# Kernel tuning notes

Measured on AMD Instinct MI355X. Metric: run time of the kernel, lower is better.

## Reference

```python
import jax, jax.numpy as jnp
import numpy as np

N_EMBD = 1024
N_HEAD = 16
HEAD_SIZE = N_EMBD // N_HEAD
B, T = 4, 2048
LN_EPS = 1e-6  # flax.linen.LayerNorm default


def _layer_norm(x, scale, bias):
    mu = jnp.mean(x, axis=-1, keepdims=True)
    var = jnp.mean(jnp.square(x - mu), axis=-1, keepdims=True)
    return (x - mu) * jax.lax.rsqrt(var + LN_EPS) * scale + bias


def setup_inputs() -> dict:
    key = jax.random.key(0)
    ks = jax.random.split(key, 12)
    s_in = 1.0 / np.sqrt(N_EMBD)
    s_ff = 1.0 / np.sqrt(4 * N_EMBD)
    return {
        "x": jax.random.normal(ks[0], (B, T, N_EMBD), jnp.float32),
        "wq": jax.random.normal(ks[1], (N_HEAD, N_EMBD, HEAD_SIZE), jnp.float32) * s_in,
        "wk": jax.random.normal(ks[2], (N_HEAD, N_EMBD, HEAD_SIZE), jnp.float32) * s_in,
        "wv": jax.random.normal(ks[3], (N_HEAD, N_EMBD, HEAD_SIZE), jnp.float32) * s_in,
        "w_proj": jax.random.normal(ks[4], (N_EMBD, N_EMBD), jnp.float32) * s_in,
        "b_proj": jnp.zeros((N_EMBD,), jnp.float32),
        "ln1_scale": jnp.ones((N_EMBD,), jnp.float32),
        "ln1_bias": jnp.zeros((N_EMBD,), jnp.float32),
        "ln2_scale": jnp.ones((N_EMBD,), jnp.float32),
        "ln2_bias": jnp.zeros((N_EMBD,), jnp.float32),
        "w1": jax.random.normal(ks[5], (N_EMBD, 4 * N_EMBD), jnp.float32) * s_in,
        "b1": jnp.zeros((4 * N_EMBD,), jnp.float32),
        "w2": jax.random.normal(ks[6], (4 * N_EMBD, N_EMBD), jnp.float32) * s_ff,
        "b2": jnp.zeros((N_EMBD,), jnp.float32),
    }


def reference(x, wq, wk, wv, w_proj, b_proj, ln1_scale, ln1_bias,
              ln2_scale, ln2_bias, w1, b1, w2, b2):
    Bb, Tt, C = x.shape
    # --- pre-LN self-attention ---
    h = _layer_norm(x, ln1_scale, ln1_bias)
    q = jnp.einsum('btc,hcd->bhtd', h, wq)
    k = jnp.einsum('btc,hcd->bhtd', h, wk)
    v = jnp.einsum('btc,hcd->bhtd', h, wv)
    # NOTE: original scales by C**-0.5 with C = full embed dim (quirk preserved)
    wei = jnp.einsum('bhtd,bhsd->bhts', q, k) * (C ** -0.5)
    tril = jnp.tril(jnp.ones((Tt, Tt), dtype=bool))
    wei = jnp.where(tril, wei, -jnp.inf)
    wei = jax.nn.softmax(wei, axis=-1)
    attn = jnp.einsum('bhts,bhsd->bhtd', wei, v)  # (B,H,T,hd)
    attn = attn.transpose(0, 2, 1, 3).reshape(Bb, Tt, -1)  # concat heads
    x = x + attn @ w_proj + b_proj
    # --- pre-LN feed-forward (dropout deterministic -> identity) ---
    h2 = _layer_norm(x, ln2_scale, ln2_bias)
    x = x + jax.nn.relu(h2 @ w1 + b1) @ w2 + b2
    return x
```

## Files before the change

kernel.cpp:

```cpp
#include <hip/hip_runtime.h>
#include <hip/hip_bf16.h>

#define BB 4
#define TT 2048
#define CC 1024
#define HH 16
#define DD 64
#define FF 4096
#define MM (BB*TT)

typedef __attribute__((ext_vector_type(4))) float  f32x4;
typedef __attribute__((ext_vector_type(8))) __bf16 bf16x8v;
typedef __attribute__((ext_vector_type(4))) short  s16x4;
typedef __attribute__((ext_vector_type(8))) short  s16x8;
typedef __attribute__((ext_vector_type(4))) unsigned short u16x4;

__device__ inline unsigned short bf16bits(float f){
  __hip_bfloat16 h = __float2bfloat16(f);
  return __builtin_bit_cast(unsigned short, h);
}
__device__ inline bf16x8v as_bf16x8(s16x8 s){ return __builtin_bit_cast(bf16x8v, s); }

__device__ inline void gload_lds16(const void* g, void* l){
  __builtin_amdgcn_global_load_lds((const __attribute__((address_space(1))) void*)g,
                                   (__attribute__((address_space(3))) void*)l, 16, 0, 0);
}

__global__ __launch_bounds__(256) void transpose_cast(const float* __restrict__ in,
                                                      unsigned short* __restrict__ out,
                                                      int K, int N){
  __shared__ float tile[32][33];
  int n0 = blockIdx.x*32, k0 = blockIdx.y*32;
  int tx = threadIdx.x, ty = threadIdx.y;
#pragma unroll
  for (int i=0;i<32;i+=8) tile[ty+i][tx] = in[(size_t)(k0+ty+i)*N + n0+tx];
  __syncthreads();
#pragma unroll
  for (int i=0;i<32;i+=8)
    out[(size_t)(n0+ty+i)*K + k0+tx] = bf16bits(tile[tx][ty+i]);
}

__global__ __launch_bounds__(256) void tcast_qkv(const float* __restrict__ wq,
                                                 const float* __restrict__ wk,
                                                 const float* __restrict__ wv,
                                                 unsigned short* __restrict__ out){
  int z = blockIdx.z; int sel = z>>4; int h = z&15;
  const float* w = (sel==0)?wq:((sel==1)?wk:wv);
  const float* in = w + (size_t)h*CC*DD;
  unsigned short* o = out + (size_t)(sel*1024 + h*64)*CC;
  __shared__ float tile[32][33];
  int d0 = blockIdx.x*32, c0 = blockIdx.y*32;
  int tx = threadIdx.x, ty = threadIdx.y;
#pragma unroll
  for (int i=0;i<32;i+=8) tile[ty+i][tx] = in[(size_t)(c0+ty+i)*DD + d0+tx];
  __syncthreads();
#pragma unroll
  for (int i=0;i<32;i+=8)
    o[(size_t)(d0+ty+i)*CC + c0+tx] = bf16bits(tile[tx][ty+i]);
}

__global__ __launch_bounds__(256) void ln_kernel(const float* __restrict__ x,
                                                 const float* __restrict__ sc,
                                                 const float* __restrict__ bi,
                                                 unsigned short* __restrict__ out){
  __shared__ float red[4];
  const int row = blockIdx.x, tid = threadIdx.x;
  const float4 xv = ((const float4*)(x + (size_t)row*CC))[tid];
  float s = xv.x + xv.y + xv.z + xv.w;
#pragma unroll
  for (int m=32;m>=1;m>>=1) s += __shfl_xor(s, m);
  if ((tid&63)==0) red[tid>>6] = s;
  __syncthreads();
  s = red[0]+red[1]+red[2]+red[3];
  const float mu = s * (1.0f/1024.0f);
  const float d0=xv.x-mu, d1=xv.y-mu, d2=xv.z-mu, d3=xv.w-mu;
  float sq = d0*d0 + d1*d1 + d2*d2 + d3*d3;
  __syncthreads();
#pragma unroll
  for (int m=32;m>=1;m>>=1) sq += __shfl_xor(sq, m);
  if ((tid&63)==0) red[tid>>6] = sq;
  __syncthreads();
  sq = red[0]+red[1]+red[2]+red[3];
  const float inv = rsqrtf(sq*(1.0f/1024.0f) + 1e-6f);
  const float4 scv = ((const float4*)sc)[tid];
  const float4 biv = ((const float4*)bi)[tid];
  u16x4 o;
  o[0] = bf16bits(d0*inv*scv.x + biv.x);
  o[1] = bf16bits(d1*inv*scv.y + biv.y);
  o[2] = bf16bits(d2*inv*scv.z + biv.z);
  o[3] = bf16bits(d3*inv*scv.w + biv.w);
  ((u16x4*)(out + (size_t)row*CC))[tid] = o;
}

template<int EPI>
__global__ __launch_bounds__(256) void gemm_bf16(
    const unsigned short* __restrict__ A, const unsigned short* __restrict__ Bt,
    void* __restrict__ Cout, const float* __restrict__ bias,
    const float* __restrict__ resid, int M, int N, int K)
{
  __shared__ unsigned short smem[8192];
  const int tid = threadIdx.x;
  const int lane = tid & 63, w = tid >> 6;
  const int m0 = blockIdx.y * 128, n0 = blockIdx.x * 128;
  const int wr = w >> 1, wc = w & 1;
  const int g = lane >> 4, q = lane & 15;
  f32x4 acc[4][4] = {};

  for (int k0 = 0; k0 < K; k0 += 32){
    __syncthreads();
#pragma unroll
    for (int i=0;i<2;i++){
      const int chunk = w*2 + i;
      const int row = chunk*16 + (lane>>2);
      const int ce  = (lane&3)*8;
      gload_lds16(A  + (size_t)(m0+row)*K + k0 + ce, (void*)&smem[chunk*512]);
      gload_lds16(Bt + (size_t)(n0+row)*K + k0 + ce, (void*)&smem[4096 + chunk*512]);
    }
    __syncthreads();
    bf16x8v af[4], bfr[4];
#pragma unroll
    for (int m=0;m<4;m++) af[m]  = as_bf16x8(*(const s16x8*)&smem[(wr*64 + m*16 + q)*32 + g*8]);
#pragma unroll
    for (int n=0;n<4;n++) bfr[n] = as_bf16x8(*(const s16x8*)&smem[4096 + (wc*64 + n*16 + q)*32 + g*8]);
#pragma unroll
    for (int m=0;m<4;m++)
#pragma unroll
      for (int n=0;n<4;n++)
        acc[m][n] = __builtin_amdgcn_mfma_f32_16x16x32_bf16(af[m], bfr[n], acc[m][n], 0,0,0);
  }

#pragma unroll
  for (int m=0;m<4;m++)
#pragma unroll
    for (int n=0;n<4;n++){
      const int col = n0 + wc*64 + n*16 + q;
#pragma unroll
      for (int r=0;r<4;r++){
        const int row = m0 + wr*64 + m*16 + g*4 + r;
        float v = acc[m][n][r];
        if (EPI==0){
          ((unsigned short*)Cout)[(size_t)row*N + col] = bf16bits(v);
        } else if (EPI==1 || EPI==3){
          v += bias[col] + resid[(size_t)row*N + col];
          ((float*)Cout)[(size_t)row*N + col] = v;
        } else {
          v += bias[col];
          v = fmaxf(v, 0.0f);
          ((unsigned short*)Cout)[(size_t)row*N + col] = bf16bits(v);
        }
      }
    }
}

__global__ __launch_bounds__(64) void attn_kernel(const unsigned short* __restrict__ qkv,
                                                  unsigned short* __restrict__ outc){
  const int lane = threadIdx.x;
  const int q0 = blockIdx.x*16;
  const int bh = blockIdx.y; const int b = bh>>4, h = bh&15;
  const int g = lane>>4, qq = lane&15;
  const size_t base = (size_t)(b*TT)*3072;
  const int qcol = h*64, kcol = 1024 + h*64, vcol = 2048 + h*64;

  s16x8 qf0, qf1;
  {
    const unsigned short* qp = qkv + base + (size_t)(q0+qq)*3072 + qcol + g*8;
    qf0 = *(const s16x8*)(qp);
    qf1 = *(const s16x8*)(qp + 32);
  }

  float m_i = -INFINITY, l_i = 0.0f;
  f32x4 ot[4] = {};

  for (int s0 = 0; s0 <= q0; s0 += 16){
    const unsigned short* kp = qkv + base + (size_t)(s0+qq)*3072 + kcol + g*8;
    s16x8 kf0 = *(const s16x8*)(kp);
    s16x8 kf1 = *(const s16x8*)(kp + 32);
    f32x4 st = {};
    st = __builtin_amdgcn_mfma_f32_16x16x32_bf16(as_bf16x8(kf0), as_bf16x8(qf0), st, 0,0,0);
    st = __builtin_amdgcn_mfma_f32_16x16x32_bf16(as_bf16x8(kf1), as_bf16x8(qf1), st, 0,0,0);
    float sv[4]; float pm = -INFINITY;
#pragma unroll
    for (int r=0;r<4;r++){
      const int s_abs = s0 + g*4 + r;
      float v = st[r] * 0.03125f;
      if (s_abs > q0 + qq) v = -INFINITY;
      sv[r] = v;
      pm = fmaxf(pm, v);
    }
    pm = fmaxf(pm, __shfl_xor(pm, 16));
    pm = fmaxf(pm, __shfl_xor(pm, 32));
    const float m_new = fmaxf(m_i, pm);
    const float alpha = __expf(m_i - m_new);
    float p[4]; float ps = 0.0f;
#pragma unroll
    for (int r=0;r<4;r++){ p[r] = __expf(sv[r] - m_new); ps += p[r]; }
    ps += __shfl_xor(ps, 16);
    ps += __shfl_xor(ps, 32);
    l_i = l_i*alpha + ps;
    s16x4 pb;
#pragma unroll
    for (int r=0;r<4;r++) pb[r] = (short)bf16bits(p[r]);
#pragma unroll
    for (int mb=0;mb<4;mb++){
      ot[mb] *= alpha;
      s16x4 vf;
#pragma unroll
      for (int j=0;j<4;j++){
        const int s_abs = s0 + g*4 + j;
        vf[j] = (short)qkv[base + (size_t)s_abs*3072 + vcol + mb*16 + qq];
      }
      ot[mb] = __builtin_amdgcn_mfma_f32_16x16x16bf16_1k(vf, pb, ot[mb], 0,0,0);
    }
    m_i = m_new;
  }

  const float inv = 1.0f / l_i;
#pragma unroll
  for (int mb=0;mb<4;mb++){
    u16x4 o;
#pragma unroll
    for (int r=0;r<4;r++) o[r] = bf16bits(ot[mb][r] * inv);
    *(u16x4*)&outc[(size_t)(b*TT + q0 + qq)*1024 + h*64 + mb*16 + g*4] = o;
  }
}

extern "C" void kernel_launch(void* const* d_in, const int* in_sizes, int n_in,
                              void* d_out, int out_size, void* d_ws, size_t ws_size,
                              hipStream_t stream)
{
  const float* x   = (const float*)d_in[0];
  const float* wq  = (const float*)d_in[1];
  const float* wk  = (const float*)d_in[2];
  const float* wv  = (const float*)d_in[3];
  const float* wpr = (const float*)d_in[4];
  const float* bpr = (const float*)d_in[5];
  const float* l1s = (const float*)d_in[6];
  const float* l1b = (const float*)d_in[7];
  const float* l2s = (const float*)d_in[8];
  const float* l2b = (const float*)d_in[9];
  const float* w1  = (const float*)d_in[10];
  const float* b1  = (const float*)d_in[11];
  const float* w2  = (const float*)d_in[12];
  const float* b2  = (const float*)d_in[13];
  float* out = (float*)d_out;

  char* ws = (char*)d_ws;
  unsigned short* qkv   = (unsigned short*)(ws + 0);
  unsigned short* hb    = (unsigned short*)(ws + 50331648);
  unsigned short* attnc = (unsigned short*)(ws + 67108864);
  float*          x1    = (float*)        (ws + 83886080);
  unsigned short* h2    = attnc;
  unsigned short* act   = (unsigned short*)(ws + 0);
  unsigned short* wqkvt = (unsigned short*)(ws + 117440512);
  unsigned short* wprt  = (unsigned short*)(ws + 123731968);
  unsigned short* w1t   = (unsigned short*)(ws + 125829120);
  unsigned short* w2t   = (unsigned short*)(ws + 134217728);

  tcast_qkv<<<dim3(2,32,48), dim3(32,8), 0, stream>>>(wq, wk, wv, wqkvt);
  transpose_cast<<<dim3(32,32),  dim3(32,8), 0, stream>>>(wpr, wprt, 1024, 1024);
  transpose_cast<<<dim3(128,32), dim3(32,8), 0, stream>>>(w1,  w1t,  1024, 4096);
  transpose_cast<<<dim3(32,128), dim3(32,8), 0, stream>>>(w2,  w2t,  4096, 1024);

  ln_kernel<<<MM, 256, 0, stream>>>(x, l1s, l1b, hb);
  gemm_bf16<0><<<dim3(24,64), 256, 0, stream>>>(hb, wqkvt, qkv, nullptr, nullptr, MM, 3072, 1024);
  attn_kernel<<<dim3(TT/16, BB*HH), 64, 0, stream>>>(qkv, attnc);
  gemm_bf16<1><<<dim3(8,64), 256, 0, stream>>>(attnc, wprt, x1, bpr, x, MM, 1024, 1024);
  ln_kernel<<<MM, 256, 0, stream>>>(x1, l2s, l2b, h2);
  gemm_bf16<2><<<dim3(32,64), 256, 0, stream>>>(h2, w1t, act, b1, nullptr, MM, 4096, 1024);
  gemm_bf16<3><<<dim3(8,64), 256, 0, stream>>>(act, w2t, out, b2, x1, MM, 1024, 4096);
}
```

Baseline: 722.1 us.

## Write V transposed from QKV GEMM, widen attention blocks, swizzle GEMM grids

The QKV GEMM epilogue now writes Q and K into a 2048-wide buffer and V transposed per batch (feature-major), so attention can load V fragments as contiguous 4-element vectors instead of scalar strided gathers. The attention kernel uses 4 waves per block (64 queries) and processes 64 keys per softmax step, amortising max/sum reductions and rescaling across four key blocks. All GEMMs get an XCD-aware block-index swizzle to improve L2 locality across chiplets. The transposed V stores are 8-byte scattered writes, which may cost some epilogue bandwidth.

```diff
diff --git a/kernel.cpp b/kernel.cpp
--- a/kernel.cpp
+++ b/kernel.cpp
@@ -92,16 +92,26 @@
   ((u16x4*)(out + (size_t)row*CC))[tid] = o;
 }
 
-template<int EPI>
+template<int EPI, int SWZ>
 __global__ __launch_bounds__(256) void gemm_bf16(
     const unsigned short* __restrict__ A, const unsigned short* __restrict__ Bt,
     void* __restrict__ Cout, const float* __restrict__ bias,
-    const float* __restrict__ resid, int M, int N, int K)
+    const float* __restrict__ resid, unsigned short* __restrict__ vT,
+    int M, int N, int K)
 {
   __shared__ unsigned short smem[8192];
   const int tid = threadIdx.x;
   const int lane = tid & 63, w = tid >> 6;
-  const int m0 = blockIdx.y * 128, n0 = blockIdx.x * 128;
+  int bx = blockIdx.x, by = blockIdx.y;
+  if (SWZ){
+    const int gx = gridDim.x;
+    const int nwg = gx * gridDim.y;
+    const int flat = bx + by*gx;
+    const int cpx = nwg >> 3;
+    const int orig = (flat & 7)*cpx + (flat >> 3);
+    bx = orig % gx; by = orig / gx;
+  }
+  const int m0 = by * 128, n0 = bx * 128;
   const int wr = w >> 1, wc = w & 1;
   const int g = lane >> 4, q = lane & 15;
   f32x4 acc[4][4] = {};
@@ -134,82 +144,112 @@
 #pragma unroll
     for (int n=0;n<4;n++){
       const int col = n0 + wc*64 + n*16 + q;
-#pragma unroll
-      for (int r=0;r<4;r++){
-        const int row = m0 + wr*64 + m*16 + g*4 + r;
-        float v = acc[m][n][r];
-        if (EPI==0){
-          ((unsigned short*)Cout)[(size_t)row*N + col] = bf16bits(v);
-        } else if (EPI==1 || EPI==3){
-          v += bias[col] + resid[(size_t)row*N + col];
-          ((float*)Cout)[(size_t)row*N + col] = v;
-        } else {
-          v += bias[col];
-          v = fmaxf(v, 0.0f);
-          ((unsigned short*)Cout)[(size_t)row*N + col] = bf16bits(v);
+      const int row0 = m0 + wr*64 + m*16 + g*4;
+      if (EPI==4 && n0 >= 2048){
+        const int c = col - 2048;
+        const int bq = row0 >> 11, t0 = row0 & 2047;
+        u16x4 o;
+#pragma unroll
+        for (int r=0;r<4;r++) o[r] = bf16bits(acc[m][n][r]);
+        *(u16x4*)&vT[((size_t)(bq*1024 + c))*2048 + t0] = o;
+      } else {
+#pragma unroll
+        for (int r=0;r<4;r++){
+          const int row = row0 + r;
+          float v = acc[m][n][r];
+          if (EPI==4){
+            ((unsigned short*)Cout)[(size_t)row*2048 + col] = bf16bits(v);
+          } else if (EPI==1 || EPI==3){
+            v += bias[col] + resid[(size_t)row*N + col];
+            ((float*)Cout)[(size_t)row*N + col] = v;
+          } else {
+            v += bias[col];
+            v = fmaxf(v, 0.0f);
+            ((unsigned short*)Cout)[(size_t)row*N + col] = bf16bits(v);
+          }
         }
       }
     }
 }
 
-__global__ __launch_bounds__(64) void attn_kernel(const unsigned short* __restrict__ qkv,
-                                                  unsigned short* __restrict__ outc){
-  const int lane = threadIdx.x;
-  const int q0 = blockIdx.x*16;
-  const int bh = blockIdx.y; const int b = bh>>4, h = bh&15;
-  const int g = lane>>4, qq = lane&15;
-  const size_t base = (size_t)(b*TT)*3072;
-  const int qcol = h*64, kcol = 1024 + h*64, vcol = 2048 + h*64;
-
-  s16x8 qf0, qf1;
-  {
-    const unsigned short* qp = qkv + base + (size_t)(q0+qq)*3072 + qcol + g*8;
-    qf0 = *(const s16x8*)(qp);
-    qf1 = *(const s16x8*)(qp + 32);
-  }
+__global__ __launch_bounds__(256) void attn_v2(const unsigned short* __restrict__ qk,
+                                               const unsigned short* __restrict__ vT,
+                                               unsigned short* __restrict__ outc){
+  const int flat = blockIdx.x + blockIdx.y*32;
+  const int orig = (flat & 7)*256 + (flat >> 3);
+  const int qt = orig & 31;
+  const int bh = orig >> 5;
+  const int b = bh >> 4, h = bh & 15;
+  const int w = threadIdx.x >> 6, lane = threadIdx.x & 63;
+  const int g = lane >> 4, qq = lane & 15;
+  const int q0 = qt*64 + w*16;
+  const size_t base = (size_t)b*TT*2048;
+
+  const unsigned short* qrow = qk + base + (size_t)(q0+qq)*2048 + h*64 + g*8;
+  const s16x8 qf0 = *(const s16x8*)qrow;
+  const s16x8 qf1 = *(const s16x8*)(qrow + 32);
+  const unsigned short* kbase = qk + base + 1024 + h*64 + g*8;
+  const size_t vbase = ((size_t)(b*1024 + h*64 + qq))*2048 + g*4;
 
   float m_i = -INFINITY, l_i = 0.0f;
   f32x4 ot[4] = {};
-
-  for (int s0 = 0; s0 <= q0; s0 += 16){
-    const unsigned short* kp = qkv + base + (size_t)(s0+qq)*3072 + kcol + g*8;
-    s16x8 kf0 = *(const s16x8*)(kp);
-    s16x8 kf1 = *(const s16x8*)(kp + 32);
-    f32x4 st = {};
-    st = __builtin_amdgcn_mfma_f32_16x16x32_bf16(as_bf16x8(kf0), as_bf16x8(qf0), st, 0,0,0);
-    st = __builtin_amdgcn_mfma_f32_16x16x32_bf16(as_bf16x8(kf1), as_bf16x8(qf1), st, 0,0,0);
-    float sv[4]; float pm = -INFINITY;
-#pragma unroll
-    for (int r=0;r<4;r++){
-      const int s_abs = s0 + g*4 + r;
-      float v = st[r] * 0.03125f;
-      if (s_abs > q0 + qq) v = -INFINITY;
-      sv[r] = v;
-      pm = fmaxf(pm, v);
+  const int smax = q0 + 15;
+
+  for (int s0 = 0; s0 <= smax; s0 += 64){
+    const int nkb = (((smax - s0) >> 4) < 3) ? ((smax - s0) >> 4) + 1 : 4;
+    float sv[4][4];
+    float pm = -INFINITY;
+#pragma unroll
+    for (int kb=0; kb<4; kb++){
+      if (kb < nkb){
+        const int sb = s0 + kb*16;
+        const unsigned short* kp = kbase + (size_t)(sb+qq)*2048;
+        const s16x8 kf0 = *(const s16x8*)kp;
+        const s16x8 kf1 = *(const s16x8*)(kp + 32);
+        f32x4 t = {};
+        t = __builtin_amdgcn_mfma_f32_16x16x32_bf16(as_bf16x8(kf0), as_bf16x8(qf0), t, 0,0,0);
+        t = __builtin_amdgcn_mfma_f32_16x16x32_bf16(as_bf16x8(kf1), as_bf16x8(qf1), t, 0,0,0);
+#pragma unroll
+        for (int r=0;r<4;r++){
+          float v = t[r] * 0.03125f;
+          if (sb + g*4 + r > q0 + qq) v = -INFINITY;
+          sv[kb][r] = v;
+          pm = fmaxf(pm, v);
+        }
+      }
     }
     pm = fmaxf(pm, __shfl_xor(pm, 16));
     pm = fmaxf(pm, __shfl_xor(pm, 32));
     const float m_new = fmaxf(m_i, pm);
     const float alpha = __expf(m_i - m_new);
-    float p[4]; float ps = 0.0f;
-#pragma unroll
-    for (int r=0;r<4;r++){ p[r] = __expf(sv[r] - m_new); ps += p[r]; }
+    float ps = 0.0f;
+    s16x4 pb[4];
+#pragma unroll
+    for (int kb=0; kb<4; kb++){
+      if (kb < nkb){
+#pragma unroll
+        for (int r=0;r<4;r++){
+          const float p = __expf(sv[kb][r] - m_new);
+          ps += p;
+          pb[kb][r] = (short)bf16bits(p);
+        }
+      }
+    }
     ps += __shfl_xor(ps, 16);
     ps += __shfl_xor(ps, 32);
     l_i = l_i*alpha + ps;
-    s16x4 pb;
-#pragma unroll
-    for (int r=0;r<4;r++) pb[r] = (short)bf16bits(p[r]);
-#pragma unroll
-    for (int mb=0;mb<4;mb++){
-      ot[mb] *= alpha;
-      s16x4 vf;
-#pragma unroll
-      for (int j=0;j<4;j++){
-        const int s_abs = s0 + g*4 + j;
-        vf[j] = (short)qkv[base + (size_t)s_abs*3072 + vcol + mb*16 + qq];
+#pragma unroll
+    for (int mb=0;mb<4;mb++) ot[mb] *= alpha;
+#pragma unroll
+    for (int kb=0; kb<4; kb++){
+      if (kb < nkb){
+        const size_t vcol = (size_t)(s0 + kb*16);
+#pragma unroll
+        for (int mb=0;mb<4;mb++){
+          const s16x4 vf = *(const s16x4*)(vT + vbase + (size_t)(mb*16)*2048 + vcol);
+          ot[mb] = __builtin_amdgcn_mfma_f32_16x16x16bf16_1k(vf, pb[kb], ot[mb], 0,0,0);
+        }
       }
-      ot[mb] = __builtin_amdgcn_mfma_f32_16x16x16bf16_1k(vf, pb, ot[mb], 0,0,0);
     }
     m_i = m_new;
   }
@@ -245,7 +285,8 @@
   float* out = (float*)d_out;
 
   char* ws = (char*)d_ws;
-  unsigned short* qkv   = (unsigned short*)(ws + 0);
+  unsigned short* qk    = (unsigned short*)(ws + 0);
+  unsigned short* vT    = (unsigned short*)(ws + 33554432);
   unsigned short* hb    = (unsigned short*)(ws + 50331648);
   unsigned short* attnc = (unsigned short*)(ws + 67108864);
   float*          x1    = (float*)        (ws + 83886080);
@@ -262,10 +303,10 @@
   transpose_cast<<<dim3(32,128), dim3(32,8), 0, stream>>>(w2,  w2t,  4096, 1024);
 
   ln_kernel<<<MM, 256, 0, stream>>>(x, l1s, l1b, hb);
-  gemm_bf16<0><<<dim3(24,64), 256, 0, stream>>>(hb, wqkvt, qkv, nullptr, nullptr, MM, 3072, 1024);
-  attn_kernel<<<dim3(TT/16, BB*HH), 64, 0, stream>>>(qkv, attnc);
-  gemm_bf16<1><<<dim3(8,64), 256, 0, stream>>>(attnc, wprt, x1, bpr, x, MM, 1024, 1024);
+  gemm_bf16<4,1><<<dim3(24,64), 256, 0, stream>>>(hb, wqkvt, qk, nullptr, nullptr, vT, MM, 3072, 1024);
+  attn_v2<<<dim3(32,64), 256, 0, stream>>>(qk, vT, attnc);
+  gemm_bf16<1,1><<<dim3(8,64), 256, 0, stream>>>(attnc, wprt, x1, bpr, x, nullptr, MM, 1024, 1024);
   ln_kernel<<<MM, 256, 0, stream>>>(x1, l2s, l2b, h2);
-  gemm_bf16<2><<<dim3(32,64), 256, 0, stream>>>(h2, w1t, act, b1, nullptr, MM, 4096, 1024);
-  gemm_bf16<3><<<dim3(8,64), 256, 0, stream>>>(act, w2t, out, b2, x1, MM, 1024, 4096);
-}
+  gemm_bf16<2,1><<<dim3(32,64), 256, 0, stream>>>(h2, w1t, act, b1, nullptr, nullptr, MM, 4096, 1024);
+  gemm_bf16<3,1><<<dim3(8,64), 256, 0, stream>>>(act, w2t, out, b2, x1, nullptr, MM, 1024, 4096);
+}
```

Result: slower. 916.4 us (+26.9%).
